# Optimization experiments

Hardware: AMD Instinct MI355X
Metric: run time of the kernel (lower is better)

## Reference

```python
import jax, jax.numpy as jnp
import numpy as np

# ---- static config (matches init_kwargs) ----
B, CIN, COUT, L = 8, 64, 64, 32768
K, STRIDE, PAD, DIL = 5, 1, 2, 1
G, DG = 4, 2                      # groups, deformable_groups_per_groups
GDG = G * DG
CD = CIN // GDG                   # channels per deformable group
DW = 7                            # depthwise kernel size of offset/mask branch
OFFSET_SCALE = 4.0
EPS = 1e-5
LOUT = (L + 2 * PAD - DIL * (K - 1) - 1) // STRIDE + 1


def setup_inputs() -> dict:
    key = jax.random.key(0)
    ks = jax.random.split(key, 8)
    s = 0.02
    f32 = jnp.float32
    return {
        "x": jax.random.normal(ks[0], (B, CIN, L), f32),
        # offset branch: depthwise conv -> per-channel groupnorm -> 1x1 conv
        "dw_off_w": (jax.random.normal(ks[1], (CIN, 1, DW), f32) * s),
        "dw_off_b": jnp.zeros((CIN,), f32),
        "gn_off_w": jnp.ones((CIN,), f32),
        "gn_off_b": jnp.zeros((CIN,), f32),
        "pw_off_w": (jax.random.normal(ks[2], (GDG * K, CIN), f32) * s),
        "pw_off_b": jnp.zeros((GDG * K,), f32),
        # attn-mask branch (same structure); final bias init to ones per repo
        "dw_m_w": (jax.random.normal(ks[3], (CIN, 1, DW), f32) * s),
        "dw_m_b": jnp.zeros((CIN,), f32),
        "gn_m_w": jnp.ones((CIN,), f32),
        "gn_m_b": jnp.zeros((CIN,), f32),
        "pw_m_w": (jax.random.normal(ks[4], (GDG * K, CIN), f32) * s),
        "pw_m_b": jnp.ones((GDG * K,), f32),
        # main conv weight (Cout, Cin/G, K) and bias, normal(0, 0.02)
        "weight": (jax.random.normal(ks[5], (COUT, CIN // G, K), f32) * s),
        "bias": (jax.random.normal(ks[6], (COUT,), f32) * s),
    }


def _dwconv(x, w, b):
    # depthwise conv1d, padding (DW-1)//2, groups = CIN
    y = jax.lax.conv_general_dilated(
        x, w, window_strides=(1,), padding=[((DW - 1) // 2, (DW - 1) // 2)],
        feature_group_count=CIN, dimension_numbers=("NCH", "OIH", "NCH"))
    return y + b[None, :, None]


def _gn_per_channel(x, g, b):
    # GroupNorm with num_groups == num_channels: normalize each channel over L
    mu = jnp.mean(x, axis=-1, keepdims=True)
    var = jnp.var(x, axis=-1, keepdims=True)
    return (x - mu) * jax.lax.rsqrt(var + EPS) * g[None, :, None] + b[None, :, None]


def _branch(x, dw_w, dw_b, gn_g, gn_b, pw_w, pw_b):
    h = _gn_per_channel(_dwconv(x, dw_w, dw_b), gn_g, gn_b)
    return jnp.einsum("oc,bcl->bol", pw_w, h) + pw_b[None, :, None]


def _deform_conv1d(x, offset, attn, weight, bias):
    # x: (B,CIN,L); offset/attn: (B,GDG*K,LOUT)
    xg = x.reshape(B, G, DG, CD, L)
    off = offset.reshape(B, G, DG, K, LOUT)
    # base sampling grid: l*stride - pad + k*dil   -> (K, LOUT)
    base = (jnp.arange(LOUT) * STRIDE - PAD)[None, :] + (jnp.arange(K) * DIL)[:, None]
    p = base.astype(x.dtype)[None, None, None] + off          # (B,G,DG,K,LOUT)
    p0 = jnp.floor(p)
    w1 = p - p0                                               # linear-interp weight
    p0i = p0.astype(jnp.int32)

    def gather(idx):
        valid = ((idx >= 0) & (idx < L)).astype(x.dtype)
        idxc = jnp.clip(idx, 0, L - 1).reshape(B, G, DG, 1, K * LOUT)
        idxc = jnp.broadcast_to(idxc, (B, G, DG, CD, K * LOUT))
        v = jnp.take_along_axis(xg, idxc, axis=-1).reshape(B, G, DG, CD, K, LOUT)
        return v * valid[:, :, :, None]

    sampled = gather(p0i) * (1.0 - w1)[:, :, :, None] + gather(p0i + 1) * w1[:, :, :, None]
    sampled = sampled * attn.reshape(B, G, DG, 1, K, LOUT)
    wg = weight.reshape(G, COUT // G, DG, CD, K)
    out = jnp.einsum("godck,bgdckl->bgol", wg, sampled).reshape(B, COUT, LOUT)
    return out + bias[None, :, None]


def reference(x, dw_off_w, dw_off_b, gn_off_w, gn_off_b, pw_off_w, pw_off_b,
              dw_m_w, dw_m_b, gn_m_w, gn_m_b, pw_m_w, pw_m_b, weight, bias):
    offset = _branch(x, dw_off_w, dw_off_b, gn_off_w, gn_off_b, pw_off_w, pw_off_b) * OFFSET_SCALE
    attn = _branch(x, dw_m_w, dw_m_b, gn_m_w, gn_m_b, pw_m_w, pw_m_b)
    # softmax modulation over the K kernel taps within each deformable group
    attn = jax.nn.softmax(attn.reshape(B, GDG, K, LOUT), axis=2).reshape(B, GDG * K, LOUT)
    return _deform_conv1d(x, offset, attn, weight, bias)
```

## Files before the change

kernel.cpp:

```cpp
#include <hip/hip_runtime.h>
#include <hip/hip_bf16.h>
#include <hip/hip_fp16.h>

typedef unsigned int   uint;
typedef unsigned short ushort;

#define NB   8
#define NC   64
#define LL   32768
#define KK   5
#define NG   4
#define NDG  2
#define NGD  8
#define NCD  8
#define NOFF 40
#define DWK  7
#define XROW (LL + 16)

typedef _Float16 f16x8 __attribute__((ext_vector_type(8)));
typedef float    f32x4 __attribute__((ext_vector_type(4)));

__device__ __forceinline__ uint pkrtz(float a, float b) {
  typedef __fp16 fp16x2n __attribute__((ext_vector_type(2)));
  fp16x2n h = __builtin_amdgcn_cvt_pkrtz(a, b);
  union { fp16x2n h; uint u; } v; v.h = h; return v.u;
}

__global__ __launch_bounds__(256) void k_prep(
    const float* __restrict__ pwA, const float* __restrict__ pwM,
    const float* __restrict__ mw,
    float* __restrict__ wtA, float* __restrict__ wtM, ushort* __restrict__ Wf)
{
  int idx = blockIdx.x * 256 + threadIdx.x;
  if (idx < 2560) {
    int c = idx / 40, o = idx % 40;
    wtA[idx] = pwA[o * NC + c];
  } else if (idx < 5120) {
    int j = idx - 2560;
    int c = j / 40, o = j % 40;
    wtM[j] = pwM[o * NC + c];
  } else if (idx < 11264) {
    int j  = idx - 5120;
    int jj = j & 7;
    int l  = (j >> 3) & 63;
    int gt = j >> 9;
    int t  = gt % 3, g = gt / 3;
    int o  = l & 15;
    int kq = t * 32 + ((l >> 4) << 3) + jj;
    float val = 0.f;
    if (kq < 80) {
      int ktap = kq >> 3, c = kq & 7;
      int d = ktap / 5, kh = ktap % 5;
      val = mw[((g * 16 + o) * 16 + d * 8 + c) * KK + kh];
    }
    Wf[j] = __half_as_ushort(__float2half(val));
  }
}

__device__ __forceinline__ void load8f(float* dst, const float* __restrict__ row,
                                       int start)
{
  if (start >= 0 && start + 8 <= LL) {
    float4 a = *(const float4*)(row + start);
    float4 b = *(const float4*)(row + start + 4);
    dst[0] = a.x; dst[1] = a.y; dst[2] = a.z; dst[3] = a.w;
    dst[4] = b.x; dst[5] = b.y; dst[6] = b.z; dst[7] = b.w;
  } else {
#pragma unroll
    for (int j = 0; j < 8; ++j) {
      int p = start + j;
      dst[j] = (p >= 0 && p < LL) ? row[p] : 0.f;
    }
  }
}

__global__ __launch_bounds__(256) void k_conv(
    const float* __restrict__ x,
    const float* __restrict__ dwAw, const float* __restrict__ dwAb,
    const float* __restrict__ dwMw, const float* __restrict__ dwMb,
    ushort* __restrict__ yA, ushort* __restrict__ yM,
    ushort* __restrict__ xT, float4* __restrict__ partial)
{
  __shared__ __align__(16) ushort lx[8 * 256];
  int tid  = threadIdx.x;
  int lblk = blockIdx.x & 127;
  int gd   = (blockIdx.x >> 7) & 7;
  int b    = blockIdx.x >> 10;
  int c    = tid >> 5;
  int q    = tid & 31;
  int l0   = lblk << 8;
  int lb   = l0 + q * 8;
  int ch   = gd * 8 + c;
  const float* row = x + (size_t)(b * NC + ch) * LL;

  float v[24];
  load8f(v + 0,  row, lb - 8);
  load8f(v + 8,  row, lb);
  load8f(v + 16, row, lb + 8);

  {
    uint4 xr;
    xr.x = pkrtz(v[8],  v[9]);
    xr.y = pkrtz(v[10], v[11]);
    xr.z = pkrtz(v[12], v[13]);
    xr.w = pkrtz(v[14], v[15]);
    *(uint4*)(lx + c * 256 + q * 8) = xr;
  }

  float wa[DWK], wm[DWK];
#pragma unroll
  for (int j = 0; j < DWK; ++j) {
    wa[j] = dwAw[ch * DWK + j];
    wm[j] = dwMw[ch * DWK + j];
  }
  float ba = dwAb[ch], bm = dwMb[ch];

  float sa = 0.f, qa = 0.f, sm = 0.f, qm = 0.f;
  float ya8[8], ym8[8];
#pragma unroll
  for (int u = 0; u < 8; ++u) {
    float ya = ba, ym = bm;
#pragma unroll
    for (int j = 0; j < DWK; ++j) {
      float xv = v[5 + u + j];
      ya += wa[j] * xv;
      ym += wm[j] * xv;
    }
    sa += ya; qa += ya * ya;
    sm += ym; qm += ym * ym;
    ya8[u] = ya; ym8[u] = ym;
  }
  uint4 pA, pM;
  pA.x = pkrtz(ya8[0], ya8[1]); pA.y = pkrtz(ya8[2], ya8[3]);
  pA.z = pkrtz(ya8[4], ya8[5]); pA.w = pkrtz(ya8[6], ya8[7]);
  pM.x = pkrtz(ym8[0], ym8[1]); pM.y = pkrtz(ym8[2], ym8[3]);
  pM.z = pkrtz(ym8[4], ym8[5]); pM.w = pkrtz(ym8[6], ym8[7]);
  *(uint4*)(yA + (size_t)(b * NC + ch) * LL + lb) = pA;
  *(uint4*)(yM + (size_t)(b * NC + ch) * LL + lb) = pM;

#pragma unroll
  for (int m = 1; m < 32; m <<= 1) {
    sa += __shfl_xor(sa, m);
    qa += __shfl_xor(qa, m);
    sm += __shfl_xor(sm, m);
    qm += __shfl_xor(qm, m);
  }
  if (q == 0)
    partial[((size_t)(b * NC + ch) << 7) + lblk] = make_float4(sa, qa, sm, qm);

  __syncthreads();
  {
    uint4 pk;
    pk.x = (uint)lx[0 * 256 + tid] | ((uint)lx[1 * 256 + tid] << 16);
    pk.y = (uint)lx[2 * 256 + tid] | ((uint)lx[3 * 256 + tid] << 16);
    pk.z = (uint)lx[4 * 256 + tid] | ((uint)lx[5 * 256 + tid] << 16);
    pk.w = (uint)lx[6 * 256 + tid] | ((uint)lx[7 * 256 + tid] << 16);
    size_t rowbase = (size_t)(b * NGD + gd) * (size_t)XROW;
    *(uint4*)(xT + (rowbase + 8 + (size_t)(l0 + tid)) * 8) = pk;
    if (tid < 8) {
      uint4 z = {0, 0, 0, 0};
      if (lblk == 0)   *(uint4*)(xT + (rowbase + tid) * 8) = z;
      if (lblk == 127) *(uint4*)(xT + (rowbase + 8 + LL + tid) * 8) = z;
    }
  }
}

__global__ __launch_bounds__(256) void k_fin(
    const float4* __restrict__ partial,
    const float* __restrict__ gnAw, const float* __restrict__ gnAb,
    const float* __restrict__ gnMw, const float* __restrict__ gnMb,
    const float* __restrict__ wtA, const float* __restrict__ wtM,
    const float* __restrict__ pbA, const float* __restrict__ pbM,
    ushort* __restrict__ wFp, float* __restrict__ biasPt)
{
  __shared__ float4 pr[256];
  __shared__ float gA[64], cA[64], gM[64], cM[64];
  __shared__ float sbA[40], sbM[40];
  int b = blockIdx.x;
  int t = threadIdx.x;
  {
    int c = t & 63, seg = t >> 6;
    const float4* pp = partial + ((size_t)(b * NC + c) << 7);
    float4 s = make_float4(0.f, 0.f, 0.f, 0.f);
    for (int i = seg; i < 128; i += 4) {
      float4 u = pp[i];
      s.x += u.x; s.y += u.y; s.z += u.z; s.w += u.w;
    }
    pr[t] = s;
  }
  __syncthreads();
  if (t < 64) {
    float4 a0 = pr[t], a1 = pr[t + 64], a2 = pr[t + 128], a3 = pr[t + 192];
    float sx = a0.x + a1.x + a2.x + a3.x;
    float sy = a0.y + a1.y + a2.y + a3.y;
    float sz = a0.z + a1.z + a2.z + a3.z;
    float sw = a0.w + a1.w + a2.w + a3.w;
    float mua = sx / LL, vara = sy / LL - mua * mua;
    float mum = sz / LL, varm = sw / LL - mum * mum;
    float ga = gnAw[t] * rsqrtf(vara + 1e-5f);
    float gm = gnMw[t] * rsqrtf(varm + 1e-5f);
    gA[t] = ga; cA[t] = gnAb[t] - mua * ga;
    gM[t] = gm; cM[t] = gnMb[t] - mum * gm;
  }
  __syncthreads();
  if (t < 40) {
    float sA = 0.f, sM = 0.f;
    for (int c = 0; c < 64; ++c) {
      sA += wtA[c * 40 + t] * cA[c];
      sM += wtM[c * 40 + t] * cM[c];
    }
    sbA[t] = 4.f * (pbA[t] + sA);
    sbM[t] = pbM[t] + sM;
  }
  for (int idx = t; idx < 8192; idx += 256) {
    int br = idx >> 12;
    int e  = idx & 4095;
    int g  = e >> 10;
    int ks = (e >> 9) & 1;
    int ln = (e >> 3) & 63;
    int j  = e & 7;
    int rr = ln & 15;
    int c  = ks * 32 + ((ln >> 4) << 3) + j;
    float v = 0.f;
    if (rr < 10) {
      int o = 10 * g + rr;
      v = br ? wtM[c * 40 + o] * gM[c] : 4.f * wtA[c * 40 + o] * gA[c];
    }
    wFp[(size_t)b * 8192 + idx] = __half_as_ushort(__float2half(v));
  }
  __syncthreads();
  if (t < 128) {
    int br = t >> 6, g = (t >> 4) & 3, m = t & 15;
    float v = 0.f;
    if (m < 10) v = br ? sbM[10 * g + m] : sbA[10 * g + m];
    biasPt[b * 128 + t] = v;
  }
}

__global__ __launch_bounds__(256) void k_pd(
    const ushort* __restrict__ yA, const ushort* __restrict__ yM,
    const ushort* __restrict__ xT,
    const ushort* __restrict__ wFp, const float* __restrict__ biasPt,
    const ushort* __restrict__ Wf, const float* __restrict__ bias,
    float* __restrict__ out)
{
  __shared__ __align__(16) char S[4 * 12288];
  int tid = threadIdx.x;
  int w   = tid >> 6;
  int ln  = tid & 63;
  int h   = ln >> 4;
  int col = ln & 15;
  int b   = blockIdx.x >> 9;
  int lb0 = (blockIdx.x & 511) << 6;

  {
    const ushort* srcA = yA + (size_t)b * NC * LL + lb0;
    const ushort* srcM = yM + (size_t)b * NC * LL + lb0;
#pragma unroll
    for (int i = 0; i < 4; ++i) {
      int fid = i * 256 + tid;
      int c = fid >> 4, qc = fid & 15;
      uint2 vA = *(const uint2*)(srcA + (size_t)c * LL + qc * 4);
      uint2 vM = *(const uint2*)(srcM + (size_t)c * LL + qc * 4);
      uint4 wv;
      wv.x = __builtin_amdgcn_perm(vM.x, vA.x, 0x05040100u);
      wv.y = __builtin_amdgcn_perm(vM.x, vA.x, 0x07060302u);
      wv.z = __builtin_amdgcn_perm(vM.y, vA.y, 0x05040100u);
      wv.w = __builtin_amdgcn_perm(vM.y, vA.y, 0x07060302u);
      *(uint4*)(S + c * 256 + ((qc << 4) ^ (((c >> 3) & 3) << 6))) = wv;
    }
  }

  const uint4* wFb = (const uint4*)(wFp + (size_t)b * 8192);
  f16x8 afA[2], afM[2];
#pragma unroll
  for (int ks = 0; ks < 2; ++ks) {
    union { uint4 u; f16x8 v; } cvA, cvM;
    cvA.u = wFb[(w * 2 + ks) * 64 + ln];
    cvM.u = wFb[512 + (w * 2 + ks) * 64 + ln];
    afA[ks] = cvA.v; afM[ks] = cvM.v;
  }
  f32x4 accA[4], accM[4];
  {
    float4 bvA = *(const float4*)(biasPt + b * 128 + w * 16 + h * 4);
    float4 bvM = *(const float4*)(biasPt + b * 128 + 64 + w * 16 + h * 4);
#pragma unroll
    for (int nt = 0; nt < 4; ++nt) {
      accA[nt][0]=bvA.x; accA[nt][1]=bvA.y; accA[nt][2]=bvA.z; accA[nt][3]=bvA.w;
      accM[nt][0]=bvM.x; accM[nt][1]=bvM.y; accM[nt][2]=bvM.z; accM[nt][3]=bvM.w;
    }
  }
  __syncthreads();

#pragma unroll
  for (int nt = 0; nt < 4; ++nt) {
#pragma unroll
    for (int ks = 0; ks < 2; ++ks) {
      const char* gp = S + (ks * 32 + h * 8) * 256
                     + ((((nt * 16 + col) << 2)) ^ (h << 6));
      uint r0 = *(const uint*)(gp + 0 * 256);
      uint r1 = *(const uint*)(gp + 1 * 256);
      uint r2 = *(const uint*)(gp + 2 * 256);
      uint r3 = *(const uint*)(gp + 3 * 256);
      uint r4 = *(const uint*)(gp + 4 * 256);
      uint r5 = *(const uint*)(gp + 5 * 256);
      uint r6 = *(const uint*)(gp + 6 * 256);
      uint r7 = *(const uint*)(gp + 7 * 256);
      union { uint u[4]; f16x8 v; } bA, bM;
      bA.u[0] = __builtin_amdgcn_perm(r1, r0, 0x05040100u);
      bA.u[1] = __builtin_amdgcn_perm(r3, r2, 0x05040100u);
      bA.u[2] = __builtin_amdgcn_perm(r5, r4, 0x05040100u);
      bA.u[3] = __builtin_amdgcn_perm(r7, r6, 0x05040100u);
      bM.u[0] = __builtin_amdgcn_perm(r1, r0, 0x07060302u);
      bM.u[1] = __builtin_amdgcn_perm(r3, r2, 0x07060302u);
      bM.u[2] = __builtin_amdgcn_perm(r5, r4, 0x07060302u);
      bM.u[3] = __builtin_amdgcn_perm(r7, r6, 0x07060302u);
      accA[nt] = __builtin_amdgcn_mfma_f32_16x16x32_f16(afA[ks], bA.v,
                                                        accA[nt], 0, 0, 0);
      accM[nt] = __builtin_amdgcn_mfma_f32_16x16x32_f16(afM[ks], bM.v,
                                                        accM[nt], 0, 0, 0);
    }
  }
  __syncthreads();

  char* wb = S + w * 12288;
#pragma unroll
  for (int r = 0; r < 4; ++r) {
    int s = h * 4 + r;
    if (s < 10) {
#pragma unroll
      for (int nt = 0; nt < 4; ++nt) {
        int pos = nt * 16 + col;
        *(float*)(wb + (s << 8) + (pos << 2)) = accA[nt][r];
        *(float*)(wb + 2560 + (s << 8) + (pos << 2)) = accM[nt][r];
      }
    }
  }
  float off[10], lg[10];
#pragma unroll
  for (int s = 0; s < 10; ++s) {
    off[s] = *(const float*)(wb + (s << 8) + (ln << 2));
    lg[s]  = *(const float*)(wb + 2560 + (s << 8) + (ln << 2));
  }
  float at[10];
  {
    float m0 = fmaxf(fmaxf(fmaxf(lg[0], lg[1]), fmaxf(lg[2], lg[3])), lg[4]);
    float m1 = fmaxf(fmaxf(fmaxf(lg[5], lg[6]), fmaxf(lg[7], lg[8])), lg[9]);
    float e[10], s0 = 0.f, s1 = 0.f;
#pragma unroll
    for (int j = 0; j < 5; ++j) { e[j] = __expf(lg[j] - m0); s0 += e[j]; }
#pragma unroll
    for (int j = 5; j < 10; ++j) { e[j] = __expf(lg[j] - m1); s1 += e[j]; }
    float r0 = 1.f / s0, r1 = 1.f / s1;
#pragma unroll
    for (int j = 0; j < 5; ++j)  at[j] = e[j] * r0;
#pragma unroll
    for (int j = 5; j < 10; ++j) at[j] = e[j] * r1;
  }

  int g = w;
  int l = lb0 + ln;

  f16x8 af[3];
#pragma unroll
  for (int t = 0; t < 3; ++t) {
    union { uint4 u; f16x8 hh; } cv;
    cv.u = ((const uint4*)Wf)[(g * 3 + t) * 64 + ln];
    af[t] = cv.hh;
  }
  int orow = (ln >> 4) << 2;
  float4 b4 = *(const float4*)(bias + g * 16 + orow);
  f32x4 acc[4];
#pragma unroll
  for (int nb = 0; nb < 4; ++nb) {
    acc[nb][0] = b4.x; acc[nb][1] = b4.y; acc[nb][2] = b4.z; acc[nb][3] = b4.w;
  }

  char* sb  = wb;
  int nbase = ln * 192;
  int msk   = (ln & 7) << 4;

  {
    f16x8 Z = {};
    *(f16x8*)(sb + ((nbase + 160) ^ msk)) = Z;
    *(f16x8*)(sb + ((nbase + 176) ^ msk)) = Z;
  }

#pragma unroll
  for (int d = 0; d < NDG; ++d) {
    const ushort* xr = xT + (size_t)(b * NGD + g * 2 + d) * (size_t)XROW * 8;
#pragma unroll
    for (int kh = 0; kh < KK; ++kh) {
      int s = d * KK + kh;
      float p = (float)(l - 2 + kh) + off[s];
      p = fminf(fmaxf(p, -1.f), 32768.f);
      float p0f = floorf(p);
      float w1  = p - p0f;
      int   i0  = (int)p0f;
      float f0 = (1.f - w1) * at[s];
      float f1 = w1 * at[s];
      _Float16 a0 = (_Float16)f0;
      _Float16 a1 = (_Float16)f1;
      f16x8 F0 = {a0, a0, a0, a0, a0, a0, a0, a0};
      f16x8 F1 = {a1, a1, a1, a1, a1, a1, a1, a1};
      const ushort* q = xr + (size_t)(i0 + 8) * 8;
      f16x8 X0 = *(const f16x8*)q;
      f16x8 X1 = *(const f16x8*)(q + 8);
      f16x8 S8 = X0 * F0 + X1 * F1;
      *(f16x8*)(sb + ((nbase + s * 16) ^ msk)) = S8;
    }
  }

  int rb0 = (ln & 15) * 192 + ((ln >> 4) << 4);
#pragma unroll
  for (int nb = 0; nb < 4; ++nb) {
#pragma unroll
    for (int t = 0; t < 3; ++t) {
      f16x8 bf = *(const f16x8*)(sb + ((rb0 + nb * 3072 + t * 64) ^ msk));
      acc[nb] = __builtin_amdgcn_mfma_f32_16x16x32_f16(af[t], bf, acc[nb],
                                                       0, 0, 0);
    }
  }

  float* ob = out + (size_t)(b * NC + g * 16 + orow) * LL + lb0 + (ln & 15);
#pragma unroll
  for (int nb = 0; nb < 4; ++nb) {
#pragma unroll
    for (int r = 0; r < 4; ++r)
      ob[(size_t)r * LL + (nb << 4)] = acc[nb][r];
  }
}

extern "C" void kernel_launch(void* const* d_in, const int* in_sizes, int n_in,
                              void* d_out, int out_size, void* d_ws, size_t ws_size,
                              hipStream_t stream)
{
  const float* x    = (const float*)d_in[0];
  const float* dwAw = (const float*)d_in[1];
  const float* dwAb = (const float*)d_in[2];
  const float* gnAw = (const float*)d_in[3];
  const float* gnAb = (const float*)d_in[4];
  const float* pwAw = (const float*)d_in[5];
  const float* pwAb = (const float*)d_in[6];
  const float* dwMw = (const float*)d_in[7];
  const float* dwMb = (const float*)d_in[8];
  const float* gnMw = (const float*)d_in[9];
  const float* gnMb = (const float*)d_in[10];
  const float* pwMw = (const float*)d_in[11];
  const float* pwMb = (const float*)d_in[12];
  const float* mw   = (const float*)d_in[13];
  const float* bias = (const float*)d_in[14];
  float* out = (float*)d_out;

  float* wtA = (float*)d_ws;
  float* wtM = wtA + 2560;
  ushort* Wf = (ushort*)(wtM + 2560);
  ushort* wFp = Wf + 6144;
  float* biasPt = (float*)(wFp + 65536);
  float4* partial = (float4*)(biasPt + 1024);
  ushort* yA = (ushort*)(partial + 65536);
  ushort* yM = yA + (size_t)NB * NC * LL;
  ushort* xT = yM + (size_t)NB * NC * LL;

  hipLaunchKernelGGL(k_prep, dim3(44), dim3(256), 0, stream,
                     pwAw, pwMw, mw, wtA, wtM, Wf);
  hipLaunchKernelGGL(k_conv, dim3(NB * NGD * 128), dim3(256), 0, stream,
                     x, dwAw, dwAb, dwMw, dwMb, yA, yM, xT, partial);
  hipLaunchKernelGGL(k_fin, dim3(NB), dim3(256), 0, stream,
                     partial, gnAw, gnAb, gnMw, gnMb, wtA, wtM, pwAb, pwMb,
                     wFp, biasPt);
  hipLaunchKernelGGL(k_pd, dim3(NB * 512), dim3(256), 0, stream,
                     yA, yM, xT, wFp, biasPt, Wf, bias, out);
}
```

Before: 197.5 us.

## Interleave offset/mask conv outputs, double per-block work in conv, add MFMA priority

The depthwise conv outputs for the offset and mask branches are now stored interleaved as packed half pairs in one buffer. The consumer kernel can then read them with a single 16-byte load instead of two loads followed by byte permutes. The conv kernel now processes 512 positions per block instead of 256, halving the grid and the number of partial GroupNorm statistics, and the finalize reduction is adjusted to match. s_setprio is raised around the MFMA loops in the main kernel to favour matrix issue, at the cost of more registers per thread in conv and fewer blocks for latency hiding.

```diff
diff --git a/kernel.cpp b/kernel.cpp
--- a/kernel.cpp
+++ b/kernel.cpp
@@ -74,38 +74,61 @@
   }
 }
 
+__device__ __forceinline__ void conv8(
+    const float* __restrict__ v, const float* __restrict__ wa,
+    const float* __restrict__ wm, float ba, float bm,
+    float& sa, float& qa, float& sm, float& qm,
+    uint4& y0, uint4& y1, uint4& xr)
+{
+  float ya8[8], ym8[8];
+#pragma unroll
+  for (int u = 0; u < 8; ++u) {
+    float ya = ba, ym = bm;
+#pragma unroll
+    for (int j = 0; j < DWK; ++j) {
+      float xv = v[5 + u + j];
+      ya += wa[j] * xv;
+      ym += wm[j] * xv;
+    }
+    sa += ya; qa += ya * ya;
+    sm += ym; qm += ym * ym;
+    ya8[u] = ya; ym8[u] = ym;
+  }
+  y0.x = pkrtz(ya8[0], ym8[0]); y0.y = pkrtz(ya8[1], ym8[1]);
+  y0.z = pkrtz(ya8[2], ym8[2]); y0.w = pkrtz(ya8[3], ym8[3]);
+  y1.x = pkrtz(ya8[4], ym8[4]); y1.y = pkrtz(ya8[5], ym8[5]);
+  y1.z = pkrtz(ya8[6], ym8[6]); y1.w = pkrtz(ya8[7], ym8[7]);
+  xr.x = pkrtz(v[8],  v[9]);   xr.y = pkrtz(v[10], v[11]);
+  xr.z = pkrtz(v[12], v[13]);  xr.w = pkrtz(v[14], v[15]);
+}
+
 __global__ __launch_bounds__(256) void k_conv(
     const float* __restrict__ x,
     const float* __restrict__ dwAw, const float* __restrict__ dwAb,
     const float* __restrict__ dwMw, const float* __restrict__ dwMb,
-    ushort* __restrict__ yA, ushort* __restrict__ yM,
+    uint* __restrict__ yAM,
     ushort* __restrict__ xT, float4* __restrict__ partial)
 {
-  __shared__ __align__(16) ushort lx[8 * 256];
+  __shared__ __align__(16) ushort lx[8 * 512];
   int tid  = threadIdx.x;
-  int lblk = blockIdx.x & 127;
-  int gd   = (blockIdx.x >> 7) & 7;
-  int b    = blockIdx.x >> 10;
+  int lblk = blockIdx.x & 63;
+  int gd   = (blockIdx.x >> 6) & 7;
+  int b    = blockIdx.x >> 9;
   int c    = tid >> 5;
   int q    = tid & 31;
-  int l0   = lblk << 8;
-  int lb   = l0 + q * 8;
+  int l0   = lblk << 9;
+  int lb0  = l0 + q * 8;
+  int lb1  = lb0 + 256;
   int ch   = gd * 8 + c;
   const float* row = x + (size_t)(b * NC + ch) * LL;
 
-  float v[24];
-  load8f(v + 0,  row, lb - 8);
-  load8f(v + 8,  row, lb);
-  load8f(v + 16, row, lb + 8);
-
-  {
-    uint4 xr;
-    xr.x = pkrtz(v[8],  v[9]);
-    xr.y = pkrtz(v[10], v[11]);
-    xr.z = pkrtz(v[12], v[13]);
-    xr.w = pkrtz(v[14], v[15]);
-    *(uint4*)(lx + c * 256 + q * 8) = xr;
-  }
+  float v0[24], v1[24];
+  load8f(v0 + 0,  row, lb0 - 8);
+  load8f(v0 + 8,  row, lb0);
+  load8f(v0 + 16, row, lb0 + 8);
+  load8f(v1 + 0,  row, lb1 - 8);
+  load8f(v1 + 8,  row, lb1);
+  load8f(v1 + 16, row, lb1 + 8);
 
   float wa[DWK], wm[DWK];
 #pragma unroll
@@ -116,27 +139,21 @@
   float ba = dwAb[ch], bm = dwMb[ch];
 
   float sa = 0.f, qa = 0.f, sm = 0.f, qm = 0.f;
-  float ya8[8], ym8[8];
-#pragma unroll
-  for (int u = 0; u < 8; ++u) {
-    float ya = ba, ym = bm;
-#pragma unroll
-    for (int j = 0; j < DWK; ++j) {
-      float xv = v[5 + u + j];
-      ya += wa[j] * xv;
-      ym += wm[j] * xv;
-    }
-    sa += ya; qa += ya * ya;
-    sm += ym; qm += ym * ym;
-    ya8[u] = ya; ym8[u] = ym;
-  }
-  uint4 pA, pM;
-  pA.x = pkrtz(ya8[0], ya8[1]); pA.y = pkrtz(ya8[2], ya8[3]);
-  pA.z = pkrtz(ya8[4], ya8[5]); pA.w = pkrtz(ya8[6], ya8[7]);
-  pM.x = pkrtz(ym8[0], ym8[1]); pM.y = pkrtz(ym8[2], ym8[3]);
-  pM.z = pkrtz(ym8[4], ym8[5]); pM.w = pkrtz(ym8[6], ym8[7]);
-  *(uint4*)(yA + (size_t)(b * NC + ch) * LL + lb) = pA;
-  *(uint4*)(yM + (size_t)(b * NC + ch) * LL + lb) = pM;
+  uint* yb = yAM + (size_t)(b * NC + ch) * LL;
+  {
+    uint4 y0, y1, xr;
+    conv8(v0, wa, wm, ba, bm, sa, qa, sm, qm, y0, y1, xr);
+    *(uint4*)(yb + lb0)     = y0;
+    *(uint4*)(yb + lb0 + 4) = y1;
+    *(uint4*)(lx + c * 512 + q * 8) = xr;
+  }
+  {
+    uint4 y0, y1, xr;
+    conv8(v1, wa, wm, ba, bm, sa, qa, sm, qm, y0, y1, xr);
+    *(uint4*)(yb + lb1)     = y0;
+    *(uint4*)(yb + lb1 + 4) = y1;
+    *(uint4*)(lx + c * 512 + 256 + q * 8) = xr;
+  }
 
 #pragma unroll
   for (int m = 1; m < 32; m <<= 1) {
@@ -146,22 +163,24 @@
     qm += __shfl_xor(qm, m);
   }
   if (q == 0)
-    partial[((size_t)(b * NC + ch) << 7) + lblk] = make_float4(sa, qa, sm, qm);
-
-  __syncthreads();
-  {
+    partial[((size_t)(b * NC + ch) << 6) + lblk] = make_float4(sa, qa, sm, qm);
+
+  __syncthreads();
+  size_t rowbase = (size_t)(b * NGD + gd) * (size_t)XROW;
+#pragma unroll
+  for (int half = 0; half < 2; ++half) {
+    int pos = half * 256 + tid;
     uint4 pk;
-    pk.x = (uint)lx[0 * 256 + tid] | ((uint)lx[1 * 256 + tid] << 16);
-    pk.y = (uint)lx[2 * 256 + tid] | ((uint)lx[3 * 256 + tid] << 16);
-    pk.z = (uint)lx[4 * 256 + tid] | ((uint)lx[5 * 256 + tid] << 16);
-    pk.w = (uint)lx[6 * 256 + tid] | ((uint)lx[7 * 256 + tid] << 16);
-    size_t rowbase = (size_t)(b * NGD + gd) * (size_t)XROW;
-    *(uint4*)(xT + (rowbase + 8 + (size_t)(l0 + tid)) * 8) = pk;
-    if (tid < 8) {
-      uint4 z = {0, 0, 0, 0};
-      if (lblk == 0)   *(uint4*)(xT + (rowbase + tid) * 8) = z;
-      if (lblk == 127) *(uint4*)(xT + (rowbase + 8 + LL + tid) * 8) = z;
-    }
+    pk.x = (uint)lx[0 * 512 + pos] | ((uint)lx[1 * 512 + pos] << 16);
+    pk.y = (uint)lx[2 * 512 + pos] | ((uint)lx[3 * 512 + pos] << 16);
+    pk.z = (uint)lx[4 * 512 + pos] | ((uint)lx[5 * 512 + pos] << 16);
+    pk.w = (uint)lx[6 * 512 + pos] | ((uint)lx[7 * 512 + pos] << 16);
+    *(uint4*)(xT + (rowbase + 8 + (size_t)(l0 + pos)) * 8) = pk;
+  }
+  if (tid < 8) {
+    uint4 z = {0, 0, 0, 0};
+    if (lblk == 0)  *(uint4*)(xT + (rowbase + tid) * 8) = z;
+    if (lblk == 63) *(uint4*)(xT + (rowbase + 8 + LL + tid) * 8) = z;
   }
 }
 
@@ -180,9 +199,9 @@
   int t = threadIdx.x;
   {
     int c = t & 63, seg = t >> 6;
-    const float4* pp = partial + ((size_t)(b * NC + c) << 7);
+    const float4* pp = partial + ((size_t)(b * NC + c) << 6);
     float4 s = make_float4(0.f, 0.f, 0.f, 0.f);
-    for (int i = seg; i < 128; i += 4) {
+    for (int i = seg; i < 64; i += 4) {
       float4 u = pp[i];
       s.x += u.x; s.y += u.y; s.z += u.z; s.w += u.w;
     }
@@ -238,8 +257,7 @@
 }
 
 __global__ __launch_bounds__(256) void k_pd(
-    const ushort* __restrict__ yA, const ushort* __restrict__ yM,
-    const ushort* __restrict__ xT,
+    const uint* __restrict__ yAM, const ushort* __restrict__ xT,
     const ushort* __restrict__ wFp, const float* __restrict__ biasPt,
     const ushort* __restrict__ Wf, const float* __restrict__ bias,
     float* __restrict__ out)
@@ -254,19 +272,12 @@
   int lb0 = (blockIdx.x & 511) << 6;
 
   {
-    const ushort* srcA = yA + (size_t)b * NC * LL + lb0;
-    const ushort* srcM = yM + (size_t)b * NC * LL + lb0;
+    const uint* src = yAM + (size_t)b * NC * LL + lb0;
 #pragma unroll
     for (int i = 0; i < 4; ++i) {
       int fid = i * 256 + tid;
       int c = fid >> 4, qc = fid & 15;
-      uint2 vA = *(const uint2*)(srcA + (size_t)c * LL + qc * 4);
-      uint2 vM = *(const uint2*)(srcM + (size_t)c * LL + qc * 4);
-      uint4 wv;
-      wv.x = __builtin_amdgcn_perm(vM.x, vA.x, 0x05040100u);
-      wv.y = __builtin_amdgcn_perm(vM.x, vA.x, 0x07060302u);
-      wv.z = __builtin_amdgcn_perm(vM.y, vA.y, 0x05040100u);
-      wv.w = __builtin_amdgcn_perm(vM.y, vA.y, 0x07060302u);
+      uint4 wv = *(const uint4*)(src + (size_t)c * LL + qc * 4);
       *(uint4*)(S + c * 256 + ((qc << 4) ^ (((c >> 3) & 3) << 6))) = wv;
     }
   }
@@ -292,6 +303,7 @@
   }
   __syncthreads();
 
+  __builtin_amdgcn_s_setprio(1);
 #pragma unroll
   for (int nt = 0; nt < 4; ++nt) {
 #pragma unroll
@@ -321,6 +333,7 @@
                                                         accM[nt], 0, 0, 0);
     }
   }
+  __builtin_amdgcn_s_setprio(0);
   __syncthreads();
 
   char* wb = S + w * 12288;
@@ -412,6 +425,7 @@
   }
 
   int rb0 = (ln & 15) * 192 + ((ln >> 4) << 4);
+  __builtin_amdgcn_s_setprio(1);
 #pragma unroll
   for (int nb = 0; nb < 4; ++nb) {
 #pragma unroll
@@ -421,6 +435,7 @@
                                                        0, 0, 0);
     }
   }
+  __builtin_amdgcn_s_setprio(0);
 
   float* ob = out + (size_t)(b * NC + g * 16 + orow) * LL + lb0 + (ln & 15);
 #pragma unroll
@@ -458,17 +473,16 @@
   ushort* wFp = Wf + 6144;
   float* biasPt = (float*)(wFp + 65536);
   float4* partial = (float4*)(biasPt + 1024);
-  ushort* yA = (ushort*)(partial + 65536);
-  ushort* yM = yA + (size_t)NB * NC * LL;
-  ushort* xT = yM + (size_t)NB * NC * LL;
+  uint* yAM = (uint*)(partial + 65536);
+  ushort* xT = (ushort*)(yAM + (size_t)NB * NC * LL);
 
   hipLaunchKernelGGL(k_prep, dim3(44), dim3(256), 0, stream,
                      pwAw, pwMw, mw, wtA, wtM, Wf);
-  hipLaunchKernelGGL(k_conv, dim3(NB * NGD * 128), dim3(256), 0, stream,
-                     x, dwAw, dwAb, dwMw, dwMb, yA, yM, xT, partial);
+  hipLaunchKernelGGL(k_conv, dim3(NB * NGD * 64), dim3(256), 0, stream,
+                     x, dwAw, dwAb, dwMw, dwMb, yAM, xT, partial);
   hipLaunchKernelGGL(k_fin, dim3(NB), dim3(256), 0, stream,
                      partial, gnAw, gnAb, gnMw, gnMb, wtA, wtM, pwAb, pwMb,
                      wFp, biasPt);
   hipLaunchKernelGGL(k_pd, dim3(NB * 512), dim3(256), 0, stream,
-                     yA, yM, xT, wFp, biasPt, Wf, bias, out);
-}
+                     yAM, xT, wFp, biasPt, Wf, bias, out);
+}
```

Result: no change. 197.7 us (+0.1%).

## Recompute depthwise conv in k_pd instead of storing yA/yM intermediates

Applied to the files above, without the earlier changes.

The first pass now only computes GroupNorm statistics and the transposed fp16 copy of x; it no longer writes the fp16 depthwise-conv outputs yA/yM. k_pd reloads fp32 x for its 64-channel tile, recomputes both depthwise convolutions in registers, packs them into the swizzled LDS layout, and adjusts the LDS read swizzle to match. This removes a large global write and re-read of the intermediates, at the cost of redundant depthwise arithmetic and halo reads of x in k_pd. It also raises wave priority around the MFMA loops with s_setprio.

```diff
diff --git a/kernel.cpp b/kernel.cpp
--- a/kernel.cpp
+++ b/kernel.cpp
@@ -74,11 +74,10 @@
   }
 }
 
-__global__ __launch_bounds__(256) void k_conv(
+__global__ __launch_bounds__(256) void k_stat(
     const float* __restrict__ x,
     const float* __restrict__ dwAw, const float* __restrict__ dwAb,
     const float* __restrict__ dwMw, const float* __restrict__ dwMb,
-    ushort* __restrict__ yA, ushort* __restrict__ yM,
     ushort* __restrict__ xT, float4* __restrict__ partial)
 {
   __shared__ __align__(16) ushort lx[8 * 256];
@@ -116,7 +115,6 @@
   float ba = dwAb[ch], bm = dwMb[ch];
 
   float sa = 0.f, qa = 0.f, sm = 0.f, qm = 0.f;
-  float ya8[8], ym8[8];
 #pragma unroll
   for (int u = 0; u < 8; ++u) {
     float ya = ba, ym = bm;
@@ -128,15 +126,7 @@
     }
     sa += ya; qa += ya * ya;
     sm += ym; qm += ym * ym;
-    ya8[u] = ya; ym8[u] = ym;
-  }
-  uint4 pA, pM;
-  pA.x = pkrtz(ya8[0], ya8[1]); pA.y = pkrtz(ya8[2], ya8[3]);
-  pA.z = pkrtz(ya8[4], ya8[5]); pA.w = pkrtz(ya8[6], ya8[7]);
-  pM.x = pkrtz(ym8[0], ym8[1]); pM.y = pkrtz(ym8[2], ym8[3]);
-  pM.z = pkrtz(ym8[4], ym8[5]); pM.w = pkrtz(ym8[6], ym8[7]);
-  *(uint4*)(yA + (size_t)(b * NC + ch) * LL + lb) = pA;
-  *(uint4*)(yM + (size_t)(b * NC + ch) * LL + lb) = pM;
+  }
 
 #pragma unroll
   for (int m = 1; m < 32; m <<= 1) {
@@ -238,7 +228,9 @@
 }
 
 __global__ __launch_bounds__(256) void k_pd(
-    const ushort* __restrict__ yA, const ushort* __restrict__ yM,
+    const float* __restrict__ x,
+    const float* __restrict__ dwAw, const float* __restrict__ dwAb,
+    const float* __restrict__ dwMw, const float* __restrict__ dwMb,
     const ushort* __restrict__ xT,
     const ushort* __restrict__ wFp, const float* __restrict__ biasPt,
     const ushort* __restrict__ Wf, const float* __restrict__ bias,
@@ -254,20 +246,43 @@
   int lb0 = (blockIdx.x & 511) << 6;
 
   {
-    const ushort* srcA = yA + (size_t)b * NC * LL + lb0;
-    const ushort* srcM = yM + (size_t)b * NC * LL + lb0;
+    int cc = tid >> 2;
+    int q  = tid & 3;
+    int p0 = lb0 + q * 16;
+    const float* row = x + (size_t)(b * NC + cc) * LL;
+    float v[32];
+    load8f(v + 0,  row, p0 - 8);
+    load8f(v + 8,  row, p0);
+    load8f(v + 16, row, p0 + 8);
+    load8f(v + 24, row, p0 + 16);
+    float wa[DWK], wm[DWK];
+#pragma unroll
+    for (int j = 0; j < DWK; ++j) {
+      wa[j] = dwAw[cc * DWK + j];
+      wm[j] = dwMw[cc * DWK + j];
+    }
+    float ba = dwAb[cc], bm = dwMb[cc];
+    uint wbuf[16];
+#pragma unroll
+    for (int u = 0; u < 16; ++u) {
+      float ya = ba, ym = bm;
+#pragma unroll
+      for (int j = 0; j < DWK; ++j) {
+        float xv = v[5 + u + j];
+        ya += wa[j] * xv;
+        ym += wm[j] * xv;
+      }
+      wbuf[u] = pkrtz(ya, ym);
+    }
+    int hc = (cc >> 3) & 3;
+    char* base = S + cc * 256;
+    int xr = (hc << 6) ^ ((cc & 3) << 4);
 #pragma unroll
     for (int i = 0; i < 4; ++i) {
-      int fid = i * 256 + tid;
-      int c = fid >> 4, qc = fid & 15;
-      uint2 vA = *(const uint2*)(srcA + (size_t)c * LL + qc * 4);
-      uint2 vM = *(const uint2*)(srcM + (size_t)c * LL + qc * 4);
       uint4 wv;
-      wv.x = __builtin_amdgcn_perm(vM.x, vA.x, 0x05040100u);
-      wv.y = __builtin_amdgcn_perm(vM.x, vA.x, 0x07060302u);
-      wv.z = __builtin_amdgcn_perm(vM.y, vA.y, 0x05040100u);
-      wv.w = __builtin_amdgcn_perm(vM.y, vA.y, 0x07060302u);
-      *(uint4*)(S + c * 256 + ((qc << 4) ^ (((c >> 3) & 3) << 6))) = wv;
+      wv.x = wbuf[i * 4 + 0]; wv.y = wbuf[i * 4 + 1];
+      wv.z = wbuf[i * 4 + 2]; wv.w = wbuf[i * 4 + 3];
+      *(uint4*)(base + ((q * 64 + i * 16) ^ xr)) = wv;
     }
   }
 
@@ -292,20 +307,21 @@
   }
   __syncthreads();
 
+  __builtin_amdgcn_s_setprio(1);
 #pragma unroll
   for (int nt = 0; nt < 4; ++nt) {
 #pragma unroll
     for (int ks = 0; ks < 2; ++ks) {
-      const char* gp = S + (ks * 32 + h * 8) * 256
-                     + ((((nt * 16 + col) << 2)) ^ (h << 6));
-      uint r0 = *(const uint*)(gp + 0 * 256);
-      uint r1 = *(const uint*)(gp + 1 * 256);
-      uint r2 = *(const uint*)(gp + 2 * 256);
-      uint r3 = *(const uint*)(gp + 3 * 256);
-      uint r4 = *(const uint*)(gp + 4 * 256);
-      uint r5 = *(const uint*)(gp + 5 * 256);
-      uint r6 = *(const uint*)(gp + 6 * 256);
-      uint r7 = *(const uint*)(gp + 7 * 256);
+      const char* rowb = S + (ks * 32 + h * 8) * 256;
+      int p4 = (((nt * 16 + col) << 2)) ^ (h << 6);
+      uint r0 = *(const uint*)(rowb + 0 * 256 + (p4 ^ 0));
+      uint r1 = *(const uint*)(rowb + 1 * 256 + (p4 ^ 16));
+      uint r2 = *(const uint*)(rowb + 2 * 256 + (p4 ^ 32));
+      uint r3 = *(const uint*)(rowb + 3 * 256 + (p4 ^ 48));
+      uint r4 = *(const uint*)(rowb + 4 * 256 + (p4 ^ 0));
+      uint r5 = *(const uint*)(rowb + 5 * 256 + (p4 ^ 16));
+      uint r6 = *(const uint*)(rowb + 6 * 256 + (p4 ^ 32));
+      uint r7 = *(const uint*)(rowb + 7 * 256 + (p4 ^ 48));
       union { uint u[4]; f16x8 v; } bA, bM;
       bA.u[0] = __builtin_amdgcn_perm(r1, r0, 0x05040100u);
       bA.u[1] = __builtin_amdgcn_perm(r3, r2, 0x05040100u);
@@ -321,6 +337,7 @@
                                                         accM[nt], 0, 0, 0);
     }
   }
+  __builtin_amdgcn_s_setprio(0);
   __syncthreads();
 
   char* wb = S + w * 12288;
@@ -403,15 +420,16 @@
       _Float16 a1 = (_Float16)f1;
       f16x8 F0 = {a0, a0, a0, a0, a0, a0, a0, a0};
       f16x8 F1 = {a1, a1, a1, a1, a1, a1, a1, a1};
-      const ushort* q = xr + (size_t)(i0 + 8) * 8;
-      f16x8 X0 = *(const f16x8*)q;
-      f16x8 X1 = *(const f16x8*)(q + 8);
+      const ushort* qp = xr + (size_t)(i0 + 8) * 8;
+      f16x8 X0 = *(const f16x8*)qp;
+      f16x8 X1 = *(const f16x8*)(qp + 8);
       f16x8 S8 = X0 * F0 + X1 * F1;
       *(f16x8*)(sb + ((nbase + s * 16) ^ msk)) = S8;
     }
   }
 
   int rb0 = (ln & 15) * 192 + ((ln >> 4) << 4);
+  __builtin_amdgcn_s_setprio(1);
 #pragma unroll
   for (int nb = 0; nb < 4; ++nb) {
 #pragma unroll
@@ -421,6 +439,7 @@
                                                        0, 0, 0);
     }
   }
+  __builtin_amdgcn_s_setprio(0);
 
   float* ob = out + (size_t)(b * NC + g * 16 + orow) * LL + lb0 + (ln & 15);
 #pragma unroll
@@ -458,17 +477,15 @@
   ushort* wFp = Wf + 6144;
   float* biasPt = (float*)(wFp + 65536);
   float4* partial = (float4*)(biasPt + 1024);
-  ushort* yA = (ushort*)(partial + 65536);
-  ushort* yM = yA + (size_t)NB * NC * LL;
-  ushort* xT = yM + (size_t)NB * NC * LL;
+  ushort* xT = (ushort*)(partial + 65536);
 
   hipLaunchKernelGGL(k_prep, dim3(44), dim3(256), 0, stream,
                      pwAw, pwMw, mw, wtA, wtM, Wf);
-  hipLaunchKernelGGL(k_conv, dim3(NB * NGD * 128), dim3(256), 0, stream,
-                     x, dwAw, dwAb, dwMw, dwMb, yA, yM, xT, partial);
+  hipLaunchKernelGGL(k_stat, dim3(NB * NGD * 128), dim3(256), 0, stream,
+                     x, dwAw, dwAb, dwMw, dwMb, xT, partial);
   hipLaunchKernelGGL(k_fin, dim3(NB), dim3(256), 0, stream,
                      partial, gnAw, gnAb, gnMw, gnMb, wtA, wtM, pwAb, pwMb,
                      wFp, biasPt);
   hipLaunchKernelGGL(k_pd, dim3(NB * 512), dim3(256), 0, stream,
-                     yA, yM, xT, wFp, biasPt, Wf, bias, out);
-}
+                     x, dwAw, dwAb, dwMw, dwMb, xT, wFp, biasPt, Wf, bias, out);
+}
```

Result: slower. 202.5 us (+2.5%).
